# Kernel tuning notes

Hardware: AMD Instinct MI355X
Metric: run time of the kernel (lower is better)

## Reference

```python
import jax, jax.numpy as jnp
import numpy as np

EPS = 1e-06


def setup_inputs() -> dict:
    key = jax.random.key(0)
    ks = jax.random.split(key, 8)
    B, L, n, C = 4, 4096, 4, 1024
    D = n * C
    x = jax.random.normal(ks[0], (B, L, n, C), dtype=jnp.float32)
    # learned params (phi_* are zero-init in the module; use small random for a
    # non-trivial correctness baseline)
    norm_w = jnp.ones((D,), dtype=jnp.float32)
    W_pre = 0.02 * jax.random.normal(ks[1], (n, D), dtype=jnp.float32)
    W_post = 0.02 * jax.random.normal(ks[2], (n, D), dtype=jnp.float32)
    W_res = 0.02 * jax.random.normal(ks[3], (n * n, D), dtype=jnp.float32)
    b_pre = jnp.ones((n,), dtype=jnp.float32) / n
    b_post = jnp.ones((n,), dtype=jnp.float32)
    b_res = jnp.zeros((n, n), dtype=jnp.float32)
    alpha_pre = jnp.float32(0.01)
    alpha_post = jnp.float32(0.01)
    alpha_res = jnp.float32(0.01)
    return {"x": x, "norm_w": norm_w, "W_pre": W_pre, "W_post": W_post,
            "W_res": W_res, "b_pre": b_pre, "b_post": b_post, "b_res": b_res,
            "alpha_pre": alpha_pre, "alpha_post": alpha_post, "alpha_res": alpha_res}


def _cayley(M):
    # M: [N, n, n] -> orthogonal Q = (I - S)^{-1} (I + S), S skew-symmetric part
    S = 0.5 * (M - jnp.swapaxes(M, -1, -2))
    I = jnp.eye(M.shape[-1], dtype=M.dtype)
    return jnp.linalg.solve(I - S, I + S)


def reference(x, norm_w, W_pre, W_post, W_res, b_pre, b_post, b_res,
              alpha_pre, alpha_post, alpha_res):
    B, L, n, C = x.shape
    xf = x.reshape(B * L, n * C)
    # RMSNorm over n*C
    rms = jnp.sqrt(jnp.mean(xf * xf, axis=-1, keepdims=True) + EPS)
    xn = (xf / rms) * norm_w
    # tiny projections
    H_pre = jax.nn.sigmoid(alpha_pre * (xn @ W_pre.T) + b_pre)          # [BL, n]
    H_post = 2.0 * jax.nn.sigmoid(alpha_post * (xn @ W_post.T) + b_post)  # [BL, n]
    M = (alpha_res * (xn @ W_res.T)).reshape(B * L, n, n) + b_res
    H_res = _cayley(M).reshape(B, L, n, n)
    H_pre = H_pre.reshape(B, L, n)
    H_post = H_post.reshape(B, L, n)
    # pre-mapping: aggregate streams -> [B, L, C]
    y = jnp.einsum('bln,blnc->blc', H_pre, x)
    z = y  # identity sublayer
    # post-mapping: distribute back to streams
    o = H_post[..., None] * z[:, :, None, :]                             # [B,L,n,C]
    # residual mapping: orthogonal stream mixing
    r = jnp.einsum('blmn,blnc->blmc', H_res, x)
    return r + o
```

## Files before the change

### kernel.cpp

```cpp
#include <hip/hip_runtime.h>
#include <math.h>

#define DTOT   4096
#define NTOK   16384
#define NJ     24
#define NG     25
#define DC     256
#define NCHUNK (DTOT / DC)
#define TPB    32

__global__ void prep_kernel(const float* __restrict__ Wpre,
                            const float* __restrict__ Wpost,
                            const float* __restrict__ Wres,
                            const float* __restrict__ nw,
                            float* __restrict__ Wtj) {
    int i = blockIdx.x * 256 + threadIdx.x;
    if (i >= NJ * DTOT) return;
    int j = i / DTOT;
    int d = i - j * DTOT;
    float w;
    if (j < 4)       w = Wpre [i];
    else if (j < 8)  w = Wpost[i - 4 * DTOT];
    else             w = Wres [i - 8 * DTOT];
    Wtj[i] = w * nw[d];
}

__global__ __launch_bounds__(256, 5) void dots_kernel(
        const float* __restrict__ x,
        const float* __restrict__ Wtj,
        float* __restrict__ Gpart) {
    __shared__ float wlds[NJ * DC];

    const int tid = threadIdx.x;
    const int ch  = blockIdx.y;

    {
        const float4* src = (const float4*)Wtj;
        float4* dst = (float4*)wlds;
        #pragma unroll
        for (int r = 0; r < 6; ++r) {
            int idx = r * 256 + tid;
            int j = idx >> 6;
            int f = idx & 63;
            dst[idx] = src[(size_t)j * (DTOT / 4) + ch * (DC / 4) + f];
        }
    }
    __syncthreads();

    const int w    = tid >> 6;
    const int lane = tid & 63;
    const int t8   = lane >> 3;
    const int dp   = lane & 7;
    const int tok  = blockIdx.x * TPB + w * 8 + t8;

    const float4* __restrict__ xp =
        (const float4*)(x + (size_t)tok * DTOT + ch * DC);
    const float4* __restrict__ wl4 = (const float4*)wlds;

    float acc[NG];
    #pragma unroll
    for (int j = 0; j < NG; ++j) acc[j] = 0.f;

    float4 xv = xp[dp];
    #pragma unroll
    for (int i = 0; i < 8; ++i) {
        float4 nx = xv;
        if (i < 7) nx = xp[(i + 1) * 8 + dp];
        const int base = i * 8 + dp;
        #pragma unroll
        for (int j = 0; j < NJ; ++j) {
            const float4 w4 = wl4[j * 64 + base];
            acc[j] += xv.x * w4.x + xv.y * w4.y + xv.z * w4.z + xv.w * w4.w;
        }
        acc[NG - 1] += xv.x * xv.x + xv.y * xv.y + xv.z * xv.z + xv.w * xv.w;
        xv = nx;
    }

    #pragma unroll
    for (int j = 0; j < NG; ++j) {
        float v = acc[j];
        v += __shfl_xor(v, 1, 64);
        v += __shfl_xor(v, 2, 64);
        v += __shfl_xor(v, 4, 64);
        acc[j] = v;
    }

    if (dp == 0) {
        float* gp = Gpart + (size_t)ch * NG * NTOK + tok;
        #pragma unroll
        for (int j = 0; j < NG; ++j)
            gp[(size_t)j * NTOK] = acc[j];
    }
}

__global__ __launch_bounds__(1024) void out_kernel(
        const float* __restrict__ x,
        const float* __restrict__ Gpart,
        const float* __restrict__ bpre,
        const float* __restrict__ bpost,
        const float* __restrict__ bres,
        const float* __restrict__ apre,
        const float* __restrict__ apost,
        const float* __restrict__ ares,
        float* __restrict__ out) {
    const int lane  = threadIdx.x & 63;
    const int token = (NTOK - 16 - blockIdx.x * 16) + (threadIdx.x >> 6);

    float s = 0.f;
    if (lane < NG) {
        const float* gp = Gpart + (size_t)lane * NTOK + token;
        #pragma unroll
        for (int c = 0; c < NCHUNK; ++c)
            s += gp[(size_t)c * NG * NTOK];
    }

    float g[NG];
    #pragma unroll
    for (int j = 0; j < NG; ++j) g[j] = __shfl(s, j, 64);

    const float inv = rsqrtf(g[NG-1] * (1.0f / DTOT) + 1e-6f);
    const float a_pre  = apre[0];
    const float a_post = apost[0];
    const float a_res  = ares[0];

    float hpre[4], hpost[4];
    #pragma unroll
    for (int i = 0; i < 4; ++i) {
        float z1 = a_pre  * g[i]     * inv + bpre[i];
        hpre[i]  = 1.f / (1.f + __expf(-z1));
        float z2 = a_post * g[4 + i] * inv + bpost[i];
        hpost[i] = 2.f / (1.f + __expf(-z2));
    }

    float M[4][4];
    #pragma unroll
    for (int i = 0; i < 4; ++i)
        #pragma unroll
        for (int j = 0; j < 4; ++j)
            M[i][j] = a_res * g[8 + i * 4 + j] * inv + bres[i * 4 + j];

    float A[4][8];
    #pragma unroll
    for (int i = 0; i < 4; ++i)
        #pragma unroll
        for (int j = 0; j < 4; ++j) {
            float S = 0.5f * (M[i][j] - M[j][i]);
            float I = (i == j) ? 1.f : 0.f;
            A[i][j]     = I - S;
            A[i][4 + j] = I + S;
        }
    #pragma unroll
    for (int k = 0; k < 4; ++k) {
        float pv = 1.f / A[k][k];
        #pragma unroll
        for (int c = 0; c < 8; ++c) A[k][c] *= pv;
        #pragma unroll
        for (int i = 0; i < 4; ++i) {
            if (i == k) continue;
            float f = A[i][k];
            #pragma unroll
            for (int c = 0; c < 8; ++c) A[i][c] -= f * A[k][c];
        }
    }
    float cf[16];
    #pragma unroll
    for (int m = 0; m < 4; ++m)
        #pragma unroll
        for (int n = 0; n < 4; ++n)
            cf[m * 4 + n] = A[m][4 + n] + hpost[m] * hpre[n];

    const float* xt = x + (size_t)token * DTOT;
    float* ot = out + (size_t)token * DTOT;

    #pragma unroll
    for (int cc = 0; cc < 4; ++cc) {
        const int c0 = cc * 256 + lane * 4;
        float4 xv[4];
        #pragma unroll
        for (int n = 0; n < 4; ++n)
            xv[n] = *(const float4*)(xt + n * 1024 + c0);
        #pragma unroll
        for (int m = 0; m < 4; ++m) {
            float4 o;
            o.x = cf[m*4+0] * xv[0].x; o.y = cf[m*4+0] * xv[0].y;
            o.z = cf[m*4+0] * xv[0].z; o.w = cf[m*4+0] * xv[0].w;
            #pragma unroll
            for (int n = 1; n < 4; ++n) {
                const float c = cf[m * 4 + n];
                o.x += c * xv[n].x;
                o.y += c * xv[n].y;
                o.z += c * xv[n].z;
                o.w += c * xv[n].w;
            }
            *(float4*)(ot + m * 1024 + c0) = o;
        }
    }
}

extern "C" void kernel_launch(void* const* d_in, const int* in_sizes, int n_in,
                              void* d_out, int out_size, void* d_ws, size_t ws_size,
                              hipStream_t stream) {
    const float* x     = (const float*)d_in[0];
    const float* nw    = (const float*)d_in[1];
    const float* Wpre  = (const float*)d_in[2];
    const float* Wpost = (const float*)d_in[3];
    const float* Wres  = (const float*)d_in[4];
    const float* bpre  = (const float*)d_in[5];
    const float* bpost = (const float*)d_in[6];
    const float* bres  = (const float*)d_in[7];
    const float* apre  = (const float*)d_in[8];
    const float* apost = (const float*)d_in[9];
    const float* ares  = (const float*)d_in[10];
    float* out = (float*)d_out;

    float* Wtj   = (float*)d_ws;
    float* Gpart = (float*)((char*)d_ws + (size_t)NJ * DTOT * sizeof(float));

    prep_kernel<<<(NJ * DTOT + 255) / 256, 256, 0, stream>>>(Wpre, Wpost, Wres, nw, Wtj);

    dim3 ga(NTOK / TPB, NCHUNK);
    dots_kernel<<<ga, 256, 0, stream>>>(x, Wtj, Gpart);

    out_kernel<<<NTOK / 16, 1024, 0, stream>>>(x, Gpart, bpre, bpost, bres,
                                               apre, apost, ares, out);
}
```

Measured before the change: 566.1 us.

## Register-block four tokens per thread in dots kernel, add nontemporal output stores

Each thread in the dots kernel now handles four tokens instead of one, so every weight value read from LDS is reused four times and LDS traffic per FLOP drops. The grid is reordered so the chunk index varies fastest, which keeps blocks for the same token group adjacent in scheduling. Occupancy hint is lowered to 3 to make room for the extra accumulator registers. The output kernel writes with nontemporal stores so the large output avoids polluting cache while x is re-read. The cost is higher register pressure and fewer resident waves to hide memory latency.

After: 582.7 us. 2.9% more time.

```diff
diff --git a/kernel.cpp b/kernel.cpp
--- a/kernel.cpp
+++ b/kernel.cpp
@@ -7,7 +7,10 @@
 #define NG     25
 #define DC     256
 #define NCHUNK (DTOT / DC)
-#define TPB    32
+#define TPW    32
+#define TPBK   128
+
+typedef float floatx4 __attribute__((ext_vector_type(4)));
 
 __global__ void prep_kernel(const float* __restrict__ Wpre,
                             const float* __restrict__ Wpost,
@@ -25,14 +28,15 @@
     Wtj[i] = w * nw[d];
 }
 
-__global__ __launch_bounds__(256, 5) void dots_kernel(
+__global__ __launch_bounds__(256, 3) void dots_kernel(
         const float* __restrict__ x,
         const float* __restrict__ Wtj,
         float* __restrict__ Gpart) {
     __shared__ float wlds[NJ * DC];
 
     const int tid = threadIdx.x;
-    const int ch  = blockIdx.y;
+    const int ch  = blockIdx.x;
+    const int tg  = blockIdx.y;
 
     {
         const float4* src = (const float4*)Wtj;
@@ -51,45 +55,68 @@
     const int lane = tid & 63;
     const int t8   = lane >> 3;
     const int dp   = lane & 7;
-    const int tok  = blockIdx.x * TPB + w * 8 + t8;
-
-    const float4* __restrict__ xp =
-        (const float4*)(x + (size_t)tok * DTOT + ch * DC);
+    const int tok0 = tg * TPBK + w * TPW + t8;
+
+    const float4* __restrict__ xp0 =
+        (const float4*)(x + (size_t)(tok0     ) * DTOT + ch * DC);
+    const float4* __restrict__ xp1 =
+        (const float4*)(x + (size_t)(tok0 +  8) * DTOT + ch * DC);
+    const float4* __restrict__ xp2 =
+        (const float4*)(x + (size_t)(tok0 + 16) * DTOT + ch * DC);
+    const float4* __restrict__ xp3 =
+        (const float4*)(x + (size_t)(tok0 + 24) * DTOT + ch * DC);
     const float4* __restrict__ wl4 = (const float4*)wlds;
 
-    float acc[NG];
-    #pragma unroll
-    for (int j = 0; j < NG; ++j) acc[j] = 0.f;
-
-    float4 xv = xp[dp];
+    float a0[NG], a1[NG], a2[NG], a3[NG];
+    #pragma unroll
+    for (int j = 0; j < NG; ++j) { a0[j] = 0.f; a1[j] = 0.f; a2[j] = 0.f; a3[j] = 0.f; }
+
+    float4 x0 = xp0[dp], x1 = xp1[dp], x2 = xp2[dp], x3 = xp3[dp];
+
     #pragma unroll
     for (int i = 0; i < 8; ++i) {
-        float4 nx = xv;
-        if (i < 7) nx = xp[(i + 1) * 8 + dp];
+        float4 n0 = x0, n1 = x1, n2 = x2, n3 = x3;
+        if (i < 7) {
+            const int nb = (i + 1) * 8 + dp;
+            n0 = xp0[nb]; n1 = xp1[nb]; n2 = xp2[nb]; n3 = xp3[nb];
+        }
         const int base = i * 8 + dp;
         #pragma unroll
         for (int j = 0; j < NJ; ++j) {
             const float4 w4 = wl4[j * 64 + base];
-            acc[j] += xv.x * w4.x + xv.y * w4.y + xv.z * w4.z + xv.w * w4.w;
-        }
-        acc[NG - 1] += xv.x * xv.x + xv.y * xv.y + xv.z * xv.z + xv.w * xv.w;
-        xv = nx;
+            a0[j] += x0.x * w4.x + x0.y * w4.y + x0.z * w4.z + x0.w * w4.w;
+            a1[j] += x1.x * w4.x + x1.y * w4.y + x1.z * w4.z + x1.w * w4.w;
+            a2[j] += x2.x * w4.x + x2.y * w4.y + x2.z * w4.z + x2.w * w4.w;
+            a3[j] += x3.x * w4.x + x3.y * w4.y + x3.z * w4.z + x3.w * w4.w;
+        }
+        a0[NG-1] += x0.x*x0.x + x0.y*x0.y + x0.z*x0.z + x0.w*x0.w;
+        a1[NG-1] += x1.x*x1.x + x1.y*x1.y + x1.z*x1.z + x1.w*x1.w;
+        a2[NG-1] += x2.x*x2.x + x2.y*x2.y + x2.z*x2.z + x2.w*x2.w;
+        a3[NG-1] += x3.x*x3.x + x3.y*x3.y + x3.z*x3.z + x3.w*x3.w;
+        x0 = n0; x1 = n1; x2 = n2; x3 = n3;
     }
 
     #pragma unroll
     for (int j = 0; j < NG; ++j) {
-        float v = acc[j];
-        v += __shfl_xor(v, 1, 64);
-        v += __shfl_xor(v, 2, 64);
-        v += __shfl_xor(v, 4, 64);
-        acc[j] = v;
+        float v0 = a0[j], v1 = a1[j], v2 = a2[j], v3 = a3[j];
+        v0 += __shfl_xor(v0, 1, 64); v1 += __shfl_xor(v1, 1, 64);
+        v2 += __shfl_xor(v2, 1, 64); v3 += __shfl_xor(v3, 1, 64);
+        v0 += __shfl_xor(v0, 2, 64); v1 += __shfl_xor(v1, 2, 64);
+        v2 += __shfl_xor(v2, 2, 64); v3 += __shfl_xor(v3, 2, 64);
+        v0 += __shfl_xor(v0, 4, 64); v1 += __shfl_xor(v1, 4, 64);
+        v2 += __shfl_xor(v2, 4, 64); v3 += __shfl_xor(v3, 4, 64);
+        a0[j] = v0; a1[j] = v1; a2[j] = v2; a3[j] = v3;
     }
 
     if (dp == 0) {
-        float* gp = Gpart + (size_t)ch * NG * NTOK + tok;
-        #pragma unroll
-        for (int j = 0; j < NG; ++j)
-            gp[(size_t)j * NTOK] = acc[j];
+        float* gp = Gpart + (size_t)ch * NG * NTOK + tok0;
+        #pragma unroll
+        for (int j = 0; j < NG; ++j) {
+            gp[(size_t)j * NTOK     ] = a0[j];
+            gp[(size_t)j * NTOK +  8] = a1[j];
+            gp[(size_t)j * NTOK + 16] = a2[j];
+            gp[(size_t)j * NTOK + 24] = a3[j];
+        }
     }
 }
 
@@ -181,7 +208,7 @@
             xv[n] = *(const float4*)(xt + n * 1024 + c0);
         #pragma unroll
         for (int m = 0; m < 4; ++m) {
-            float4 o;
+            floatx4 o;
             o.x = cf[m*4+0] * xv[0].x; o.y = cf[m*4+0] * xv[0].y;
             o.z = cf[m*4+0] * xv[0].z; o.w = cf[m*4+0] * xv[0].w;
             #pragma unroll
@@ -192,7 +219,7 @@
                 o.z += c * xv[n].z;
                 o.w += c * xv[n].w;
             }
-            *(float4*)(ot + m * 1024 + c0) = o;
+            __builtin_nontemporal_store(o, (floatx4*)(ot + m * 1024 + c0));
         }
     }
 }
@@ -218,7 +245,7 @@
 
     prep_kernel<<<(NJ * DTOT + 255) / 256, 256, 0, stream>>>(Wpre, Wpost, Wres, nw, Wtj);
 
-    dim3 ga(NTOK / TPB, NCHUNK);
+    dim3 ga(NCHUNK, NTOK / TPBK);
     dots_kernel<<<ga, 256, 0, stream>>>(x, Wtj, Gpart);
 
     out_kernel<<<NTOK / 16, 1024, 0, stream>>>(x, Gpart, bpre, bpost, bres,
```
